# Optimization experiments

Hardware: AMD Instinct MI355X
Metric: run time of the kernel (lower is better)

## Reference

```python
import math
import jax, jax.numpy as jnp
import numpy as np

EMBED_SIZE = 768
HEAD_SIZE = 64


def setup_inputs() -> dict:
    key = jax.random.key(0)
    kx, kq, kk, kv = jax.random.split(key, 4)
    B, S = 4, 4096
    s = 1.0 / math.sqrt(EMBED_SIZE)
    x = jax.random.normal(kx, (B, S, EMBED_SIZE), dtype=jnp.float32)
    # nn.Linear(embed, head, bias=False): y = x @ W.T with W [head, embed]
    Wq = jax.random.uniform(kq, (HEAD_SIZE, EMBED_SIZE), dtype=jnp.float32, minval=-s, maxval=s)
    Wk = jax.random.uniform(kk, (HEAD_SIZE, EMBED_SIZE), dtype=jnp.float32, minval=-s, maxval=s)
    Wv = jax.random.uniform(kv, (HEAD_SIZE, EMBED_SIZE), dtype=jnp.float32, minval=-s, maxval=s)
    return {"x": x, "Wq": Wq, "Wk": Wk, "Wv": Wv}


def reference(x, Wq, Wk, Wv):
    # q,k,v: [B, S, H]
    q = jnp.einsum("bse,he->bsh", x, Wq)
    k = jnp.einsum("bse,he->bsh", x, Wk)
    v = jnp.einsum("bse,he->bsh", x, Wv)
    # NOTE: original uses `//` (floor division) by sqrt(head_size)
    scores = jnp.floor(jnp.einsum("bqh,bkh->bqk", q, k) / math.sqrt(HEAD_SIZE))
    attn = jax.nn.softmax(scores, axis=-1)
    return jnp.einsum("bqk,bkh->bqh", attn, v)
```

## Files before the change

kernel.cpp:

```cpp
#include <hip/hip_runtime.h>
#include <math.h>
#include <stdint.h>

#define B 4
#define S 4096
#define E 768
#define H 64
#define NMAT 192

typedef _Float16 half_t;
typedef __attribute__((ext_vector_type(8))) _Float16 half8;
typedef __attribute__((ext_vector_type(4))) _Float16 half4;
typedef __attribute__((ext_vector_type(4))) float f32x4;

#define LOG2E 1.4426950408889634f

__global__ __launch_bounds__(256) void wprep_kernel(
    const float* __restrict__ Wq, const float* __restrict__ Wk,
    const float* __restrict__ Wv, half_t* __restrict__ Wst)
{
    int gid = blockIdx.x * 256 + threadIdx.x;
    int m = gid / (H * E);
    int rem = gid - m * (H * E);
    int h = rem / E;
    int e = rem - h * E;
    const float* W = (m == 0) ? Wq : (m == 1) ? Wk : Wv;
    float val = W[h * E + e];
    half_t hi = (half_t)val;
    float lo = val - (float)hi;
    int n = m * H + h;
    int ks = e >> 5, kk = e & 31;
    size_t base = ((size_t)(ks * NMAT + n) * 2) * 32 + kk;
    Wst[base]      = hi;
    Wst[base + 32] = (half_t)lo;
}

#define WPAD 40
__global__ __launch_bounds__(512) void proj_kernel(
    const float* __restrict__ x, const half_t* __restrict__ Wst,
    half_t* __restrict__ qhi, half_t* __restrict__ qlo,
    half_t* __restrict__ khi, half_t* __restrict__ klo,
    half_t* __restrict__ vt)
{
    __shared__ __align__(16) half_t W_s[NMAT * 2 * WPAD];

    const int t = threadIdx.x;
    const int w = t >> 6, lane = t & 63;
    const int col = lane & 15, quad = lane >> 4;
    const int nsplit = w & 3, msub = w >> 2;
    const int mrow = blockIdx.x * 32 + msub * 16 + col;

    f32x4 acc[3];
    #pragma unroll
    for (int i = 0; i < 3; ++i) acc[i] = (f32x4){0.f, 0.f, 0.f, 0.f};

    for (int ks = 0; ks < 24; ++ks) {
        __syncthreads();
        if (t < NMAT * 2) {
            const half_t* src = Wst + ((size_t)ks * NMAT * 2 + t) * 32;
            half_t* dst = W_s + t * WPAD;
            *(half8*)(dst)      = *(const half8*)(src);
            *(half8*)(dst + 8)  = *(const half8*)(src + 8);
            *(half8*)(dst + 16) = *(const half8*)(src + 16);
            *(half8*)(dst + 24) = *(const half8*)(src + 24);
        }
        __syncthreads();

        const float* xp = x + (size_t)mrow * E + ks * 32 + quad * 8;
        float4 xa = *(const float4*)xp;
        float4 xb = *(const float4*)(xp + 4);
        float xv[8] = {xa.x, xa.y, xa.z, xa.w, xb.x, xb.y, xb.z, xb.w};
        half8 ah, al;
        #pragma unroll
        for (int j = 0; j < 8; ++j) {
            half_t hi = (half_t)xv[j];
            ah[j] = hi;
            al[j] = (half_t)(xv[j] - (float)hi);
        }

        #pragma unroll
        for (int ci = 0; ci < 3; ++ci) {
            int c = nsplit + ci * 4;
            const half_t* wr = W_s + (size_t)(c * 16 + col) * (2 * WPAD);
            half8 bh = *(const half8*)(wr + quad * 8);
            half8 bl = *(const half8*)(wr + WPAD + quad * 8);
            acc[ci] = __builtin_amdgcn_mfma_f32_16x16x32_f16(ah, bh, acc[ci], 0, 0, 0);
            acc[ci] = __builtin_amdgcn_mfma_f32_16x16x32_f16(al, bh, acc[ci], 0, 0, 0);
            acc[ci] = __builtin_amdgcn_mfma_f32_16x16x32_f16(ah, bl, acc[ci], 0, 0, 0);
        }
    }

    const int srow0 = blockIdx.x * 32 + msub * 16 + quad * 4;
    const int hcol = nsplit * 16 + col;
    #pragma unroll
    for (int r = 0; r < 4; ++r) {
        int srow = srow0 + r;
        float vq = acc[0][r];
        half_t hq = (half_t)vq;
        qhi[(size_t)srow * H + hcol] = hq;
        qlo[(size_t)srow * H + hcol] = (half_t)(vq - (float)hq);
        float vk = acc[1][r];
        half_t hk = (half_t)vk;
        khi[(size_t)srow * H + hcol] = hk;
        klo[(size_t)srow * H + hcol] = (half_t)(vk - (float)hk);
    }
    {
        half4 pk;
        #pragma unroll
        for (int r = 0; r < 4; ++r) pk[r] = (half_t)acc[2][r];
        int bb = srow0 >> 12, s0 = srow0 & (S - 1);
        *(half4*)(vt + ((size_t)(bb * H + hcol)) * S + s0) = pk;
    }
}

#define KPAD 72
#define VPAD 136
#define PPAD 40

__global__ __launch_bounds__(512) void flash_kernel(
    const half_t* __restrict__ qhi, const half_t* __restrict__ qlo,
    const half_t* __restrict__ khi, const half_t* __restrict__ klo,
    const half_t* __restrict__ vt, float* __restrict__ out)
{
    __shared__ __align__(16) char smem[64512];
    half_t* kh_s = (half_t*)smem;
    half_t* kl_s = kh_s + 128 * KPAD;
    half_t* vt_s = kl_s + 128 * KPAD;
    half_t* p_s  = vt_s + 64 * VPAD;

    const int t = threadIdx.x;
    const int w = t >> 6, lane = t & 63;
    const int col = lane & 15, quad = lane >> 4;
    const int qt = w & 1, ksw = w >> 1;
    const int b = blockIdx.x >> 7;
    const int qtile = blockIdx.x & 127;
    const int qrow0 = b * S + qtile * 32 + qt * 16;

    half8 qh[2], ql[2];
    #pragma unroll
    for (int ks = 0; ks < 2; ++ks) {
        size_t off = (size_t)(qrow0 + col) * H + ks * 32 + quad * 8;
        qh[ks] = *(const half8*)(qhi + off);
        ql[ks] = *(const half8*)(qlo + off);
    }

    f32x4 O[4];
    #pragma unroll
    for (int d = 0; d < 4; ++d) O[d] = (f32x4){0.f, 0.f, 0.f, 0.f};
    float l[4] = {0.f, 0.f, 0.f, 0.f};

    const half_t* kh_g = khi + (size_t)b * S * H;
    const half_t* kl_g = klo + (size_t)b * S * H;
    const half_t* vt_g = vt  + (size_t)b * H * S;

    const int skey = t >> 2;
    const int sch  = (t & 3) * 16;
    const int vdim = t >> 3;
    const int vch  = (t & 7) * 16;
    half_t* pw = p_s + w * 16 * PPAD;
    const int k0 = ksw * 32;

    for (int kt = 0; kt < 32; ++kt) {
        __syncthreads();
        {
            size_t goff = (size_t)(kt * 128 + skey) * H + sch;
            *(half8*)(kh_s + skey * KPAD + sch)     = *(const half8*)(kh_g + goff);
            *(half8*)(kh_s + skey * KPAD + sch + 8) = *(const half8*)(kh_g + goff + 8);
            *(half8*)(kl_s + skey * KPAD + sch)     = *(const half8*)(kl_g + goff);
            *(half8*)(kl_s + skey * KPAD + sch + 8) = *(const half8*)(kl_g + goff + 8);
            size_t voff = (size_t)vdim * S + kt * 128 + vch;
            *(half8*)(vt_s + vdim * VPAD + vch)     = *(const half8*)(vt_g + voff);
            *(half8*)(vt_s + vdim * VPAD + vch + 8) = *(const half8*)(vt_g + voff + 8);
        }
        __syncthreads();

        #pragma unroll
        for (int nt = 0; nt < 2; ++nt) {
            f32x4 a = (f32x4){0.f, 0.f, 0.f, 0.f};
            const half_t* kr = kh_s + (k0 + nt * 16 + col) * KPAD;
            const half_t* lr = kl_s + (k0 + nt * 16 + col) * KPAD;
            #pragma unroll
            for (int ks = 0; ks < 2; ++ks) {
                half8 bh = *(const half8*)(kr + ks * 32 + quad * 8);
                half8 bl = *(const half8*)(lr + ks * 32 + quad * 8);
                a = __builtin_amdgcn_mfma_f32_16x16x32_f16(qh[ks], bh, a, 0, 0, 0);
                a = __builtin_amdgcn_mfma_f32_16x16x32_f16(ql[ks], bh, a, 0, 0, 0);
                a = __builtin_amdgcn_mfma_f32_16x16x32_f16(qh[ks], bl, a, 0, 0, 0);
            }
            #pragma unroll
            for (int r = 0; r < 4; ++r) {
                float s = floorf(a[r] * 0.125f);
                float p = exp2f((s - 8.0f) * LOG2E);
                l[r] += p;
                pw[(quad * 4 + r) * PPAD + nt * 16 + col] = (half_t)p;
            }
        }

        half8 pf = *(const half8*)(pw + col * PPAD + quad * 8);
        #pragma unroll
        for (int d = 0; d < 4; ++d) {
            half8 vf = *(const half8*)(vt_s + (d * 16 + col) * VPAD + k0 + quad * 8);
            O[d] = __builtin_amdgcn_mfma_f32_16x16x32_f16(pf, vf, O[d], 0, 0, 0);
        }
    }

    #pragma unroll
    for (int mask = 1; mask <= 8; mask <<= 1) {
        #pragma unroll
        for (int r = 0; r < 4; ++r) l[r] += __shfl_xor(l[r], mask);
    }

    __syncthreads();
    float* Oc  = (float*)smem;
    float* l_s = (float*)(smem + 32768);
    #pragma unroll
    for (int d = 0; d < 4; ++d) {
        #pragma unroll
        for (int r = 0; r < 4; ++r)
            Oc[((w * 16) + quad * 4 + r) * 64 + d * 16 + col] = O[d][r];
    }
    if (col == 0) {
        #pragma unroll
        for (int r = 0; r < 4; ++r) l_s[w * 16 + quad * 4 + r] = l[r];
    }
    __syncthreads();

    {
        int row = t >> 4;
        int d0 = (t & 15) * 4;
        int qtl = row >> 4, r16 = row & 15;
        float den = 0.f;
        float num0 = 0.f, num1 = 0.f, num2 = 0.f, num3 = 0.f;
        #pragma unroll
        for (int ks = 0; ks < 4; ++ks) {
            int wi = ks * 2 + qtl;
            den += l_s[wi * 16 + r16];
            const float* oc = Oc + (size_t)(wi * 16 + r16) * 64 + d0;
            num0 += oc[0]; num1 += oc[1]; num2 += oc[2]; num3 += oc[3];
        }
        float4 o;
        o.x = num0 / den; o.y = num1 / den; o.z = num2 / den; o.w = num3 / den;
        *(float4*)(out + (size_t)(b * S + qtile * 32 + row) * H + d0) = o;
    }
}

extern "C" void kernel_launch(void* const* d_in, const int* in_sizes, int n_in,
                              void* d_out, int out_size, void* d_ws, size_t ws_size,
                              hipStream_t stream) {
    const float* x  = (const float*)d_in[0];
    const float* Wq = (const float*)d_in[1];
    const float* Wk = (const float*)d_in[2];
    const float* Wv = (const float*)d_in[3];
    float* outp = (float*)d_out;

    const size_t N = (size_t)B * S * H;
    half_t* qhi = (half_t*)d_ws;
    half_t* qlo = qhi + N;
    half_t* khi = qlo + N;
    half_t* klo = khi + N;
    half_t* vt  = klo + N;
    half_t* Wst = vt + N;

    wprep_kernel<<<(3 * H * E) / 256, 256, 0, stream>>>(Wq, Wk, Wv, Wst);
    proj_kernel<<<(B * S) / 32, 512, 0, stream>>>(x, Wst, qhi, qlo, khi, klo, vt);
    flash_kernel<<<(B * S) / 32, 512, 0, stream>>>(qhi, qlo, khi, klo, vt, outp);
}
```

Measured before the change: 195.3 us.

## Switch attention to 32x32 MFMA tiles with double-buffered swizzled LDS and pipelined projection

The flash kernel now handles 64 query rows per block with 32x32x16 MFMAs and keeps K-hi, K-lo and V^T tiles in double-buffered, XOR-swizzled LDS. The next tile is prefetched into registers during compute, which removes one barrier per iteration. The projection kernel also double-buffers its weight tiles and drops the low-order correction MFMA for V, whose result is stored only as fp16. The aim is more reuse per K/V load, fewer barriers and fewer LDS bank conflicts, at the cost of much more LDS (about 112KB) and higher register pressure.

```diff
diff --git a/kernel.cpp b/kernel.cpp
--- a/kernel.cpp
+++ b/kernel.cpp
@@ -12,6 +12,7 @@
 typedef __attribute__((ext_vector_type(8))) _Float16 half8;
 typedef __attribute__((ext_vector_type(4))) _Float16 half4;
 typedef __attribute__((ext_vector_type(4))) float f32x4;
+typedef __attribute__((ext_vector_type(16))) float f32x16;
 
 #define LOG2E 1.4426950408889634f
 
@@ -35,14 +36,14 @@
     Wst[base + 32] = (half_t)lo;
 }
 
-#define WPAD 40
-__global__ __launch_bounds__(512) void proj_kernel(
+#define WROW 72
+__global__ __launch_bounds__(512, 4) void proj_kernel(
     const float* __restrict__ x, const half_t* __restrict__ Wst,
     half_t* __restrict__ qhi, half_t* __restrict__ qlo,
     half_t* __restrict__ khi, half_t* __restrict__ klo,
     half_t* __restrict__ vt)
 {
-    __shared__ __align__(16) half_t W_s[NMAT * 2 * WPAD];
+    __shared__ __align__(16) half_t W_s[2][NMAT * WROW];
 
     const int t = threadIdx.x;
     const int w = t >> 6, lane = t & 63;
@@ -50,21 +51,28 @@
     const int nsplit = w & 3, msub = w >> 2;
     const int mrow = blockIdx.x * 32 + msub * 16 + col;
 
+    half8 stg[4];
     f32x4 acc[3];
     #pragma unroll
     for (int i = 0; i < 3; ++i) acc[i] = (f32x4){0.f, 0.f, 0.f, 0.f};
 
+    if (t < 384) {
+        const half_t* src = Wst + ((size_t)0 * NMAT * 2 + t) * 32;
+        #pragma unroll
+        for (int i = 0; i < 4; ++i) stg[i] = *(const half8*)(src + i * 8);
+        half_t* dst = &W_s[0][(t >> 1) * WROW + (t & 1) * 32];
+        #pragma unroll
+        for (int i = 0; i < 4; ++i) *(half8*)(dst + i * 8) = stg[i];
+    }
+    __syncthreads();
+
     for (int ks = 0; ks < 24; ++ks) {
-        __syncthreads();
-        if (t < NMAT * 2) {
-            const half_t* src = Wst + ((size_t)ks * NMAT * 2 + t) * 32;
-            half_t* dst = W_s + t * WPAD;
-            *(half8*)(dst)      = *(const half8*)(src);
-            *(half8*)(dst + 8)  = *(const half8*)(src + 8);
-            *(half8*)(dst + 16) = *(const half8*)(src + 16);
-            *(half8*)(dst + 24) = *(const half8*)(src + 24);
-        }
-        __syncthreads();
+        const int cur = ks & 1;
+        if (ks < 23 && t < 384) {
+            const half_t* src = Wst + ((size_t)(ks + 1) * NMAT * 2 + t) * 32;
+            #pragma unroll
+            for (int i = 0; i < 4; ++i) stg[i] = *(const half8*)(src + i * 8);
+        }
 
         const float* xp = x + (size_t)mrow * E + ks * 32 + quad * 8;
         float4 xa = *(const float4*)xp;
@@ -81,13 +89,22 @@
         #pragma unroll
         for (int ci = 0; ci < 3; ++ci) {
             int c = nsplit + ci * 4;
-            const half_t* wr = W_s + (size_t)(c * 16 + col) * (2 * WPAD);
+            const half_t* wr = &W_s[cur][(c * 16 + col) * WROW];
             half8 bh = *(const half8*)(wr + quad * 8);
-            half8 bl = *(const half8*)(wr + WPAD + quad * 8);
             acc[ci] = __builtin_amdgcn_mfma_f32_16x16x32_f16(ah, bh, acc[ci], 0, 0, 0);
-            acc[ci] = __builtin_amdgcn_mfma_f32_16x16x32_f16(al, bh, acc[ci], 0, 0, 0);
-            acc[ci] = __builtin_amdgcn_mfma_f32_16x16x32_f16(ah, bl, acc[ci], 0, 0, 0);
-        }
+            if (ci < 2) {
+                half8 bl = *(const half8*)(wr + 32 + quad * 8);
+                acc[ci] = __builtin_amdgcn_mfma_f32_16x16x32_f16(al, bh, acc[ci], 0, 0, 0);
+                acc[ci] = __builtin_amdgcn_mfma_f32_16x16x32_f16(ah, bl, acc[ci], 0, 0, 0);
+            }
+        }
+
+        if (ks < 23 && t < 384) {
+            half_t* dst = &W_s[cur ^ 1][(t >> 1) * WROW + (t & 1) * 32];
+            #pragma unroll
+            for (int i = 0; i < 4; ++i) *(half8*)(dst + i * 8) = stg[i];
+        }
+        __syncthreads();
     }
 
     const int srow0 = blockIdx.x * 32 + msub * 16 + quad * 4;
@@ -113,134 +130,181 @@
     }
 }
 
-#define KPAD 72
-#define VPAD 136
-#define PPAD 40
-
-__global__ __launch_bounds__(512) void flash_kernel(
+__global__ __launch_bounds__(512, 2) void flash_kernel(
     const half_t* __restrict__ qhi, const half_t* __restrict__ qlo,
     const half_t* __restrict__ khi, const half_t* __restrict__ klo,
     const half_t* __restrict__ vt, float* __restrict__ out)
 {
-    __shared__ __align__(16) char smem[64512];
-    half_t* kh_s = (half_t*)smem;
-    half_t* kl_s = kh_s + 128 * KPAD;
-    half_t* vt_s = kl_s + 128 * KPAD;
-    half_t* p_s  = vt_s + 64 * VPAD;
+    __shared__ __align__(16) char smem[114688];
 
     const int t = threadIdx.x;
     const int w = t >> 6, lane = t & 63;
-    const int col = lane & 15, quad = lane >> 4;
-    const int qt = w & 1, ksw = w >> 1;
-    const int b = blockIdx.x >> 7;
-    const int qtile = blockIdx.x & 127;
-    const int qrow0 = b * S + qtile * 32 + qt * 16;
-
-    half8 qh[2], ql[2];
-    #pragma unroll
-    for (int ks = 0; ks < 2; ++ks) {
-        size_t off = (size_t)(qrow0 + col) * H + ks * 32 + quad * 8;
+    const int n32 = lane & 31, l5 = lane >> 5;
+    const int qsub = w & 1, ksw = w >> 1;
+
+    const int b = blockIdx.x >> 6;
+    const int qtile = blockIdx.x & 63;
+    const int qrow0 = b * S + qtile * 64;
+    const int wrow0 = qrow0 + qsub * 32;
+
+    half_t* p_s = (half_t*)(smem + 98304);
+
+    half8 qh[4], ql[4];
+    #pragma unroll
+    for (int ks = 0; ks < 4; ++ks) {
+        size_t off = (size_t)(wrow0 + n32) * H + ks * 16 + l5 * 8;
         qh[ks] = *(const half8*)(qhi + off);
         ql[ks] = *(const half8*)(qlo + off);
     }
 
-    f32x4 O[4];
-    #pragma unroll
-    for (int d = 0; d < 4; ++d) O[d] = (f32x4){0.f, 0.f, 0.f, 0.f};
-    float l[4] = {0.f, 0.f, 0.f, 0.f};
+    f32x16 O[2];
+    #pragma unroll
+    for (int i = 0; i < 2; ++i)
+        #pragma unroll
+        for (int r = 0; r < 16; ++r) O[i][r] = 0.f;
+    float lacc[16];
+    #pragma unroll
+    for (int r = 0; r < 16; ++r) lacc[r] = 0.f;
 
     const half_t* kh_g = khi + (size_t)b * S * H;
     const half_t* kl_g = klo + (size_t)b * S * H;
-    const half_t* vt_g = vt  + (size_t)b * H * S;
-
-    const int skey = t >> 2;
-    const int sch  = (t & 3) * 16;
-    const int vdim = t >> 3;
-    const int vch  = (t & 7) * 16;
-    half_t* pw = p_s + w * 16 * PPAD;
-    const int k0 = ksw * 32;
+    const half_t* vt_g = vt + (size_t)b * H * S;
+
+    half8 stg[6];
+
+    auto load_tile = [&](int kt) {
+        #pragma unroll
+        for (int i = 0; i < 6; ++i) {
+            int f = t + 512 * i;
+            const half_t* src;
+            if (i < 2) {
+                int keyl = f >> 3, p = f & 7, c = p ^ (keyl & 7);
+                src = kh_g + (size_t)(kt * 128 + keyl) * H + c * 8;
+            } else if (i < 4) {
+                int f2 = f - 1024;
+                int keyl = f2 >> 3, p = f2 & 7, c = p ^ (keyl & 7);
+                src = kl_g + (size_t)(kt * 128 + keyl) * H + c * 8;
+            } else {
+                int f2 = f - 2048;
+                int dim = f2 >> 4, p = f2 & 15, c = p ^ (dim & 15);
+                src = vt_g + (size_t)dim * S + kt * 128 + c * 8;
+            }
+            stg[i] = *(const half8*)src;
+        }
+    };
+    auto store_tile = [&](int buf) {
+        half_t* base = (half_t*)(smem + buf * 49152);
+        #pragma unroll
+        for (int i = 0; i < 6; ++i) {
+            int f = t + 512 * i;
+            int sec = f >> 10, f2 = f & 1023;
+            int off;
+            if (sec < 2) off = sec * 8192 + (f2 >> 3) * 64 + (f2 & 7) * 8;
+            else         off = 16384 + (f2 >> 4) * 128 + (f2 & 15) * 8;
+            *(half8*)(base + off) = stg[i];
+        }
+    };
+
+    load_tile(0);
+    store_tile(0);
+    __syncthreads();
+
+    const int keyl = ksw * 32 + n32;
+    const int pc = keyl >> 3, po = keyl & 7;
+    const int prow = qsub * 32 + n32;
 
     for (int kt = 0; kt < 32; ++kt) {
+        const int cur = kt & 1;
+        if (kt < 31) load_tile(kt + 1);
+
+        half_t* khs = (half_t*)(smem + cur * 49152);
+        half_t* kls = khs + 8192;
+        half_t* vts = kls + 8192;
+
+        f32x16 acc;
+        #pragma unroll
+        for (int r = 0; r < 16; ++r) acc[r] = 0.f;
+        #pragma unroll
+        for (int ks = 0; ks < 4; ++ks) {
+            int phys = ((ks * 2 + l5) ^ (keyl & 7)) * 8;
+            half8 bh = *(const half8*)(khs + keyl * 64 + phys);
+            half8 bl = *(const half8*)(kls + keyl * 64 + phys);
+            acc = __builtin_amdgcn_mfma_f32_32x32x16_f16(qh[ks], bh, acc, 0, 0, 0);
+            acc = __builtin_amdgcn_mfma_f32_32x32x16_f16(ql[ks], bh, acc, 0, 0, 0);
+            acc = __builtin_amdgcn_mfma_f32_32x32x16_f16(qh[ks], bl, acc, 0, 0, 0);
+        }
+
+        #pragma unroll
+        for (int r = 0; r < 16; ++r) {
+            float sc = floorf(acc[r] * 0.125f);
+            float p = exp2f((sc - 8.0f) * LOG2E);
+            lacc[r] += p;
+            int rowl = qsub * 32 + (r & 3) + 8 * (r >> 2) + 4 * l5;
+            p_s[rowl * 128 + ((pc ^ (rowl & 15)) << 3) + po] = (half_t)p;
+        }
+
+        #pragma unroll
+        for (int ks2 = 0; ks2 < 2; ++ks2) {
+            int c = ksw * 4 + ks2 * 2 + l5;
+            half8 pf = *(const half8*)(p_s + prow * 128 + ((c ^ (prow & 15)) << 3));
+            #pragma unroll
+            for (int nct = 0; nct < 2; ++nct) {
+                int dim = nct * 32 + n32;
+                half8 vf = *(const half8*)(vts + dim * 128 + ((c ^ (dim & 15)) << 3));
+                O[nct] = __builtin_amdgcn_mfma_f32_32x32x16_f16(pf, vf, O[nct], 0, 0, 0);
+            }
+        }
+
+        if (kt < 31) store_tile(cur ^ 1);
         __syncthreads();
-        {
-            size_t goff = (size_t)(kt * 128 + skey) * H + sch;
-            *(half8*)(kh_s + skey * KPAD + sch)     = *(const half8*)(kh_g + goff);
-            *(half8*)(kh_s + skey * KPAD + sch + 8) = *(const half8*)(kh_g + goff + 8);
-            *(half8*)(kl_s + skey * KPAD + sch)     = *(const half8*)(kl_g + goff);
-            *(half8*)(kl_s + skey * KPAD + sch + 8) = *(const half8*)(kl_g + goff + 8);
-            size_t voff = (size_t)vdim * S + kt * 128 + vch;
-            *(half8*)(vt_s + vdim * VPAD + vch)     = *(const half8*)(vt_g + voff);
-            *(half8*)(vt_s + vdim * VPAD + vch + 8) = *(const half8*)(vt_g + voff + 8);
-        }
-        __syncthreads();
-
-        #pragma unroll
-        for (int nt = 0; nt < 2; ++nt) {
-            f32x4 a = (f32x4){0.f, 0.f, 0.f, 0.f};
-            const half_t* kr = kh_s + (k0 + nt * 16 + col) * KPAD;
-            const half_t* lr = kl_s + (k0 + nt * 16 + col) * KPAD;
-            #pragma unroll
-            for (int ks = 0; ks < 2; ++ks) {
-                half8 bh = *(const half8*)(kr + ks * 32 + quad * 8);
-                half8 bl = *(const half8*)(lr + ks * 32 + quad * 8);
-                a = __builtin_amdgcn_mfma_f32_16x16x32_f16(qh[ks], bh, a, 0, 0, 0);
-                a = __builtin_amdgcn_mfma_f32_16x16x32_f16(ql[ks], bh, a, 0, 0, 0);
-                a = __builtin_amdgcn_mfma_f32_16x16x32_f16(qh[ks], bl, a, 0, 0, 0);
-            }
-            #pragma unroll
-            for (int r = 0; r < 4; ++r) {
-                float s = floorf(a[r] * 0.125f);
-                float p = exp2f((s - 8.0f) * LOG2E);
-                l[r] += p;
-                pw[(quad * 4 + r) * PPAD + nt * 16 + col] = (half_t)p;
-            }
-        }
-
-        half8 pf = *(const half8*)(pw + col * PPAD + quad * 8);
-        #pragma unroll
-        for (int d = 0; d < 4; ++d) {
-            half8 vf = *(const half8*)(vt_s + (d * 16 + col) * VPAD + k0 + quad * 8);
-            O[d] = __builtin_amdgcn_mfma_f32_16x16x32_f16(pf, vf, O[d], 0, 0, 0);
-        }
-    }
-
-    #pragma unroll
-    for (int mask = 1; mask <= 8; mask <<= 1) {
-        #pragma unroll
-        for (int r = 0; r < 4; ++r) l[r] += __shfl_xor(l[r], mask);
-    }
-
+    }
+
+    #pragma unroll
+    for (int mask = 1; mask <= 16; mask <<= 1) {
+        #pragma unroll
+        for (int r = 0; r < 16; ++r) lacc[r] += __shfl_xor(lacc[r], mask);
+    }
+
+    float* Oc  = (float*)smem;
+    float* l_s = (float*)(smem + 65536);
+    #pragma unroll
+    for (int nct = 0; nct < 2; ++nct) {
+        #pragma unroll
+        for (int r = 0; r < 16; ++r) {
+            int rowl = qsub * 32 + (r & 3) + 8 * (r >> 2) + 4 * l5;
+            Oc[(ksw * 64 + rowl) * 64 + nct * 32 + n32] = O[nct][r];
+        }
+    }
+    if (n32 == 0) {
+        #pragma unroll
+        for (int r = 0; r < 16; ++r) {
+            int rowl = qsub * 32 + (r & 3) + 8 * (r >> 2) + 4 * l5;
+            l_s[ksw * 64 + rowl] = lacc[r];
+        }
+    }
     __syncthreads();
-    float* Oc  = (float*)smem;
-    float* l_s = (float*)(smem + 32768);
-    #pragma unroll
-    for (int d = 0; d < 4; ++d) {
-        #pragma unroll
-        for (int r = 0; r < 4; ++r)
-            Oc[((w * 16) + quad * 4 + r) * 64 + d * 16 + col] = O[d][r];
-    }
-    if (col == 0) {
-        #pragma unroll
-        for (int r = 0; r < 4; ++r) l_s[w * 16 + quad * 4 + r] = l[r];
-    }
-    __syncthreads();
 
     {
-        int row = t >> 4;
-        int d0 = (t & 15) * 4;
-        int qtl = row >> 4, r16 = row & 15;
+        int row = t >> 3;
+        int d0 = (t & 7) * 8;
         float den = 0.f;
-        float num0 = 0.f, num1 = 0.f, num2 = 0.f, num3 = 0.f;
-        #pragma unroll
-        for (int ks = 0; ks < 4; ++ks) {
-            int wi = ks * 2 + qtl;
-            den += l_s[wi * 16 + r16];
-            const float* oc = Oc + (size_t)(wi * 16 + r16) * 64 + d0;
-            num0 += oc[0]; num1 += oc[1]; num2 += oc[2]; num3 += oc[3];
-        }
-        float4 o;
-        o.x = num0 / den; o.y = num1 / den; o.z = num2 / den; o.w = num3 / den;
-        *(float4*)(out + (size_t)(b * S + qtile * 32 + row) * H + d0) = o;
+        float4 na = make_float4(0.f, 0.f, 0.f, 0.f);
+        float4 nb = make_float4(0.f, 0.f, 0.f, 0.f);
+        #pragma unroll
+        for (int k = 0; k < 4; ++k) {
+            den += l_s[k * 64 + row];
+            const float* oc = Oc + (size_t)(k * 64 + row) * 64 + d0;
+            float4 a = *(const float4*)oc;
+            float4 bq = *(const float4*)(oc + 4);
+            na.x += a.x;  na.y += a.y;  na.z += a.z;  na.w += a.w;
+            nb.x += bq.x; nb.y += bq.y; nb.z += bq.z; nb.w += bq.w;
+        }
+        float inv = 1.f / den;
+        float4 o1 = make_float4(na.x * inv, na.y * inv, na.z * inv, na.w * inv);
+        float4 o2 = make_float4(nb.x * inv, nb.y * inv, nb.z * inv, nb.w * inv);
+        float* op = out + (size_t)(qrow0 + row) * H + d0;
+        *(float4*)op = o1;
+        *(float4*)(op + 4) = o2;
     }
 }
 
@@ -263,5 +327,5 @@
 
     wprep_kernel<<<(3 * H * E) / 256, 256, 0, stream>>>(Wq, Wk, Wv, Wst);
     proj_kernel<<<(B * S) / 32, 512, 0, stream>>>(x, Wst, qhi, qlo, khi, klo, vt);
-    flash_kernel<<<(B * S) / 32, 512, 0, stream>>>(qhi, qlo, khi, klo, vt, outp);
+    flash_kernel<<<B * (S / 64), 512, 0, stream>>>(qhi, qlo, khi, klo, vt, outp);
 }
```

After: 177.4 us. 1.1x faster.
